# Performance work log

Measured on AMD Instinct MI355X. Metric: run time of the kernel, lower is better.

Reference implementation:

```python
import jax, jax.numpy as jnp
import numpy as np

E, TOP_K = 8, 2          # num_experts, num_experts_per_tok
B, S, H, I = 4, 2048, 1024, 4096  # batch, seq, hidden, intermediate
STD = 0.02


def setup_inputs() -> dict:
    key = jax.random.key(0)
    k0, k1, k2, k3 = jax.random.split(key, 4)
    return {
        "x": jax.random.normal(k0, (B, S, H), jnp.float32),
        "w_gate": jax.random.normal(k1, (E, H), jnp.float32) * STD,                 # gate: Linear(H->E, no bias)
        "w_fc": jax.random.normal(k2, (E, I, H), jnp.float32) * STD,                # c_fc per-expert [E, out, in]
        "b_fc": jnp.zeros((E, I), jnp.float32),
        "w_proj": jax.random.normal(k3, (E, H, I), jnp.float32) * (STD / np.sqrt(2 * 24)),  # c_proj, n_layer=24 init scale
        "b_proj": jnp.zeros((E, H), jnp.float32),
    }


def reference(x, w_gate, w_fc, b_fc, w_proj, b_proj):
    b, s, h = x.shape
    xf = x.reshape(-1, h)                       # [T, H], T = B*S
    T = xf.shape[0]

    # --- routing (softmax in fp32, top-k, renormalize) ---
    router_logits = xf @ w_gate.T               # [T, E]
    probs = jax.nn.softmax(router_logits.astype(jnp.float32), axis=-1)
    top_w, top_idx = jax.lax.top_k(probs, TOP_K)            # [T, K]
    top_w = top_w / jnp.sum(top_w, axis=-1, keepdims=True)  # normalize_expert_weights
    top_w = top_w.astype(x.dtype)

    # combine[t, e] = gate weight of expert e for token t (0 if not selected)
    combine = jnp.zeros((T, E), x.dtype).at[jnp.arange(T)[:, None], top_idx].add(top_w)

    # --- experts: weighted sum of per-expert MLPs (same math as sort/gather/scatter) ---
    out = jnp.zeros_like(xf)
    for e in range(E):
        ht = jax.nn.gelu(xf @ w_fc[e].T + b_fc[e], approximate=False)  # [T, I]
        ht = ht @ w_proj[e].T + b_proj[e]                              # [T, H]
        out = out + combine[:, e:e + 1] * ht

    return out.reshape(b, s, h), router_logits
```

## Files before the change

### kernel.cpp

```cpp
#include <hip/hip_runtime.h>
#include <hip/hip_bf16.h>
#include <math.h>

#define T_TOK 8192
#define HID 1024
#define IDIM 4096
#define NE 8
#define TK (T_TOK*2)

typedef __attribute__((ext_vector_type(8))) short short8;
typedef __attribute__((ext_vector_type(4))) float f32x4;

__device__ __forceinline__ void gld_lds16(const void* g, void* l)
{
    __builtin_amdgcn_global_load_lds(
        (const __attribute__((address_space(1))) void*)g,
        (__attribute__((address_space(3))) void*)l, 16, 0, 0);
}

__global__ __launch_bounds__(256) void cvt_kernel(const float* __restrict__ src,
                                                  __hip_bfloat16* __restrict__ dst, int n4)
{
    int i = blockIdx.x * 256 + threadIdx.x;
    int stride = gridDim.x * 256;
    for (; i < n4; i += stride) {
        float4 v = ((const float4*)src)[i];
        union { __hip_bfloat16 h[4]; ushort4 u; } t;
        t.h[0] = __float2bfloat16(v.x);
        t.h[1] = __float2bfloat16(v.y);
        t.h[2] = __float2bfloat16(v.z);
        t.h[3] = __float2bfloat16(v.w);
        ((ushort4*)dst)[i] = t.u;
    }
}

__global__ __launch_bounds__(256) void router_kernel(const float* __restrict__ x,
                                                     const float* __restrict__ wg,
                                                     float* __restrict__ logits_out,
                                                     int* __restrict__ top_idx,
                                                     float* __restrict__ top_w,
                                                     int* __restrict__ counts)
{
    int wave = threadIdx.x >> 6, lane = threadIdx.x & 63;
    int t = blockIdx.x * 4 + wave;
    const float* xr = x + (size_t)t * HID;
    float acc[NE];
#pragma unroll
    for (int e = 0; e < NE; e++) acc[e] = 0.f;
    for (int h = lane; h < HID; h += 64) {
        float xv = xr[h];
#pragma unroll
        for (int e = 0; e < NE; e++) acc[e] += xv * wg[e * HID + h];
    }
#pragma unroll
    for (int e = 0; e < NE; e++)
        for (int off = 32; off > 0; off >>= 1)
            acc[e] += __shfl_down(acc[e], off, 64);
    if (lane == 0) {
        float mx = acc[0];
        for (int e = 1; e < NE; e++) mx = fmaxf(mx, acc[e]);
        float p[NE]; float s = 0.f;
        for (int e = 0; e < NE; e++) { p[e] = expf(acc[e] - mx); s += p[e]; }
        for (int e = 0; e < NE; e++) logits_out[(size_t)t * NE + e] = acc[e];
        int i1 = 0;
        for (int e = 1; e < NE; e++) if (p[e] > p[i1]) i1 = e;
        int i2 = -1;
        for (int e = 0; e < NE; e++) { if (e == i1) continue; if (i2 < 0 || p[e] > p[i2]) i2 = e; }
        float w1 = p[i1], w2 = p[i2], sw = w1 + w2;
        top_idx[t * 2] = i1; top_idx[t * 2 + 1] = i2;
        top_w[t * 2] = w1 / sw; top_w[t * 2 + 1] = w2 / sw;
        atomicAdd(&counts[i1], 1);
        atomicAdd(&counts[i2], 1);
    }
}

__global__ void scan_kernel(const int* __restrict__ counts, int* __restrict__ offsets)
{
    if (threadIdx.x == 0) {
        int s = 0;
        for (int e = 0; e < NE; e++) { offsets[e] = s; s += counts[e]; }
        offsets[NE] = s;
    }
}

__global__ __launch_bounds__(256) void scatter_kernel(const int* __restrict__ top_idx,
                                                      const float* __restrict__ top_w,
                                                      const int* __restrict__ offsets,
                                                      int* __restrict__ counts2,
                                                      int* __restrict__ expert_tok,
                                                      float* __restrict__ slot_w,
                                                      int* __restrict__ slot_of)
{
    int t = blockIdx.x * 256 + threadIdx.x;
    if (t >= T_TOK) return;
    for (int k = 0; k < 2; k++) {
        int e = top_idx[t * 2 + k];
        int pos = atomicAdd(&counts2[e], 1);
        int slot = offsets[e] + pos;
        expert_tok[slot] = t;
        slot_w[slot] = top_w[t * 2 + k];
        slot_of[t * 2 + k] = slot;
    }
}

__global__ __launch_bounds__(256) void gather_kernel(const float* __restrict__ x,
                                                     const int* __restrict__ expert_tok,
                                                     __hip_bfloat16* __restrict__ xg)
{
    int slot = blockIdx.x;
    int tok = expert_tok[slot];
    const float4* src = (const float4*)(x + (size_t)tok * HID);
    ushort4* dst = (ushort4*)(xg + (size_t)slot * HID);
    int h = threadIdx.x;
    float4 v = src[h];
    union { __hip_bfloat16 h4[4]; ushort4 u; } t;
    t.h4[0] = __float2bfloat16(v.x);
    t.h4[1] = __float2bfloat16(v.y);
    t.h4[2] = __float2bfloat16(v.z);
    t.h4[3] = __float2bfloat16(v.w);
    dst[h] = t.u;
}

template <int KDIM>
__device__ __forceinline__ void moe_gemm_loop(const __hip_bfloat16* __restrict__ A,
                                              int m0, int cnt,
                                              const __hip_bfloat16* __restrict__ B,
                                              __hip_bfloat16* Alds, __hip_bfloat16* Blds,
                                              f32x4 (&acc)[4][4])
{
    const int tid = threadIdx.x;
    const int lane = tid & 63, wave = tid >> 6;
    const int wt = (wave & 1) * 64, wn = (wave >> 1) * 64;
    const int fm = lane & 15, q = lane >> 4;
    const int csw = (q ^ ((fm >> 1) & 3)) * 8;

    const int srow = wave * 32 + (lane >> 2);
    const int cg = ((lane & 3) ^ ((lane >> 3) & 3)) * 8;
    int ra0 = m0 + srow;      ra0 = (ra0 < cnt) ? ra0 : (cnt - 1);
    int ra1 = m0 + srow + 16; ra1 = (ra1 < cnt) ? ra1 : (cnt - 1);
    const __hip_bfloat16* gA0 = A + (size_t)ra0 * KDIM + cg;
    const __hip_bfloat16* gA1 = A + (size_t)ra1 * KDIM + cg;
    const __hip_bfloat16* gB0 = B + (size_t)srow * KDIM + cg;
    const __hip_bfloat16* gB1 = B + (size_t)(srow + 16) * KDIM + cg;
    __hip_bfloat16* lA0 = Alds + (wave * 32) * 32;
    __hip_bfloat16* lA1 = lA0 + 16 * 32;
    __hip_bfloat16* lB0 = Blds + (wave * 32) * 32;
    __hip_bfloat16* lB1 = lB0 + 16 * 32;

    for (int kt = 0; kt < KDIM / 32; ++kt) {
        __syncthreads();
        gld_lds16(gA0, lA0); gld_lds16(gA1, lA1);
        gld_lds16(gB0, lB0); gld_lds16(gB1, lB1);
        gA0 += 32; gA1 += 32; gB0 += 32; gB1 += 32;
        __syncthreads();

        short8 tf[4], wf[4];
#pragma unroll
        for (int mi = 0; mi < 4; mi++)
            tf[mi] = *(const short8*)&Alds[(wt + mi * 16 + fm) * 32 + csw];
#pragma unroll
        for (int ni = 0; ni < 4; ni++)
            wf[ni] = *(const short8*)&Blds[(wn + ni * 16 + fm) * 32 + csw];
#pragma unroll
        for (int mi = 0; mi < 4; mi++)
#pragma unroll
            for (int ni = 0; ni < 4; ni++)
                acc[mi][ni] = __builtin_amdgcn_mfma_f32_16x16x32_bf16(
                    wf[ni], tf[mi], acc[mi][ni], 0, 0, 0);
    }
}

__global__ __launch_bounds__(256) void gemm_fc_kernel(const __hip_bfloat16* __restrict__ xg,
                                                      const __hip_bfloat16* __restrict__ wfc,
                                                      const float* __restrict__ b_fc,
                                                      const int* __restrict__ offsets,
                                                      __hip_bfloat16* __restrict__ ht)
{
    __shared__ __hip_bfloat16 Alds[128 * 32];
    __shared__ __hip_bfloat16 Blds[128 * 32];
    const int e = blockIdx.z;
    const int off = offsets[e];
    const int cnt = offsets[e + 1] - off;
    const int m0 = blockIdx.y * 128;
    if (m0 >= cnt) return;
    const int n0 = blockIdx.x * 128;

    f32x4 acc[4][4] = {};
    moe_gemm_loop<HID>(xg + (size_t)off * HID, m0, cnt,
                       wfc + (size_t)e * IDIM * HID + (size_t)n0 * HID, Alds, Blds, acc);

    const int tid = threadIdx.x, lane = tid & 63, wave = tid >> 6;
    const int wt = (wave & 1) * 64, wn = (wave >> 1) * 64, fm = lane & 15, q = lane >> 4;
#pragma unroll
    for (int mi = 0; mi < 4; mi++) {
        int m = m0 + wt + mi * 16 + fm;
        if (m >= cnt) continue;
        __hip_bfloat16* row = ht + (size_t)(off + m) * IDIM + n0 + wn;
#pragma unroll
        for (int ni = 0; ni < 4; ni++) {
            int nb = ni * 16 + q * 4;
            float4 bias = *(const float4*)&b_fc[(size_t)e * IDIM + n0 + wn + nb];
            union { __hip_bfloat16 h[4]; ushort4 u; } t;
#pragma unroll
            for (int r = 0; r < 4; r++) {
                float v = acc[mi][ni][r] + ((const float*)&bias)[r];
                t.h[r] = __float2bfloat16(0.5f * v * (1.0f + erff(v * 0.70710678118654752f)));
            }
            *(ushort4*)&row[nb] = t.u;
        }
    }
}

__global__ __launch_bounds__(256) void gemm_proj_kernel(const __hip_bfloat16* __restrict__ ht,
                                                        const __hip_bfloat16* __restrict__ wproj,
                                                        const float* __restrict__ b_proj,
                                                        const int* __restrict__ offsets,
                                                        const float* __restrict__ slot_w,
                                                        __hip_bfloat16* __restrict__ contrib)
{
    __shared__ __hip_bfloat16 Alds[128 * 32];
    __shared__ __hip_bfloat16 Blds[128 * 32];
    const int f = blockIdx.x;
    const int x = f & 7, j = (f >> 3) & 7, H = f >> 6;
    const int G = H * 8 + x;
    const int e = G >> 6, mb = G & 63, nbk = j;
    const int off = offsets[e];
    const int cnt = offsets[e + 1] - off;
    const int m0 = mb * 128;
    if (m0 >= cnt) return;
    const int n0 = nbk * 128;

    f32x4 acc[4][4] = {};
    moe_gemm_loop<IDIM>(ht + (size_t)off * IDIM, m0, cnt,
                        wproj + (size_t)e * HID * IDIM + (size_t)n0 * IDIM, Alds, Blds, acc);

    const int tid = threadIdx.x, lane = tid & 63, wave = tid >> 6;
    const int wt = (wave & 1) * 64, wn = (wave >> 1) * 64, fm = lane & 15, q = lane >> 4;
#pragma unroll
    for (int mi = 0; mi < 4; mi++) {
        int m = m0 + wt + mi * 16 + fm;
        if (m >= cnt) continue;
        float sw = slot_w[off + m];
        __hip_bfloat16* row = contrib + (size_t)(off + m) * HID + n0 + wn;
#pragma unroll
        for (int ni = 0; ni < 4; ni++) {
            int nb = ni * 16 + q * 4;
            float4 bias = *(const float4*)&b_proj[(size_t)e * HID + n0 + wn + nb];
            union { __hip_bfloat16 h[4]; ushort4 u; } t;
#pragma unroll
            for (int r = 0; r < 4; r++) {
                float v = (acc[mi][ni][r] + ((const float*)&bias)[r]) * sw;
                t.h[r] = __float2bfloat16(v);
            }
            *(ushort4*)&row[nb] = t.u;
        }
    }
}

__global__ __launch_bounds__(256) void combine_kernel(const __hip_bfloat16* __restrict__ contrib,
                                                      const int* __restrict__ slot_of,
                                                      float* __restrict__ out)
{
    int t = blockIdx.x;
    int s0 = slot_of[t * 2], s1 = slot_of[t * 2 + 1];
    const ushort4* c0 = (const ushort4*)(contrib + (size_t)s0 * HID);
    const ushort4* c1 = (const ushort4*)(contrib + (size_t)s1 * HID);
    float4* o = (float4*)(out + (size_t)t * HID);
    int h = threadIdx.x;
    ushort4 a = c0[h], b = c1[h];
    union { unsigned u; float f; } f0, f1, f2, f3, g0, g1, g2, g3;
    f0.u = ((unsigned)a.x << 16); f1.u = ((unsigned)a.y << 16);
    f2.u = ((unsigned)a.z << 16); f3.u = ((unsigned)a.w << 16);
    g0.u = ((unsigned)b.x << 16); g1.u = ((unsigned)b.y << 16);
    g2.u = ((unsigned)b.z << 16); g3.u = ((unsigned)b.w << 16);
    float4 r;
    r.x = f0.f + g0.f; r.y = f1.f + g1.f; r.z = f2.f + g2.f; r.w = f3.f + g3.f;
    o[h] = r;
}

extern "C" void kernel_launch(void* const* d_in, const int* in_sizes, int n_in,
                              void* d_out, int out_size, void* d_ws, size_t ws_size,
                              hipStream_t stream)
{
    const float* x      = (const float*)d_in[0];
    const float* w_gate = (const float*)d_in[1];
    const float* w_fc   = (const float*)d_in[2];
    const float* b_fc   = (const float*)d_in[3];
    const float* w_proj = (const float*)d_in[4];
    const float* b_proj = (const float*)d_in[5];
    float* out = (float*)d_out;
    float* logits_out = out + (size_t)T_TOK * HID;

    char* ws = (char*)d_ws;
    const size_t WB = (size_t)NE * IDIM * HID * 2;
    size_t o_wfc     = 0;
    size_t o_wproj   = o_wfc + WB;
    size_t o_xg      = o_wproj + WB;
    size_t o_ht      = o_xg + (size_t)TK * HID * 2;
    size_t o_contrib = o_ht + (size_t)TK * IDIM * 2;
    size_t o_route   = o_contrib + (size_t)TK * HID * 2;

    __hip_bfloat16* wfc_b   = (__hip_bfloat16*)(ws + o_wfc);
    __hip_bfloat16* wproj_b = (__hip_bfloat16*)(ws + o_wproj);
    __hip_bfloat16* xg      = (__hip_bfloat16*)(ws + o_xg);
    __hip_bfloat16* ht      = (__hip_bfloat16*)(ws + o_ht);
    __hip_bfloat16* contrib = (__hip_bfloat16*)(ws + o_contrib);

    size_t ro = o_route;
    int*   top_idx    = (int*)(ws + ro);   ro += (size_t)T_TOK * 2 * 4;
    float* top_w      = (float*)(ws + ro); ro += (size_t)T_TOK * 2 * 4;
    int*   counts     = (int*)(ws + ro);   ro += NE * 4;
    int*   counts2    = (int*)(ws + ro);   ro += NE * 4;
    int*   offsets    = (int*)(ws + ro);   ro += 16 * 4;
    int*   expert_tok = (int*)(ws + ro);   ro += (size_t)TK * 4;
    float* slot_w     = (float*)(ws + ro); ro += (size_t)TK * 4;
    int*   slot_of    = (int*)(ws + ro);   ro += (size_t)T_TOK * 2 * 4;

    if (ws_size < ro) return;

    hipMemsetAsync(counts, 0, 2 * NE * sizeof(int), stream);

    const int n4 = NE * IDIM * HID / 4;
    cvt_kernel<<<2048, 256, 0, stream>>>(w_fc, wfc_b, n4);
    cvt_kernel<<<2048, 256, 0, stream>>>(w_proj, wproj_b, n4);

    router_kernel<<<T_TOK / 4, 256, 0, stream>>>(x, w_gate, logits_out, top_idx, top_w, counts);
    scan_kernel<<<1, 64, 0, stream>>>(counts, offsets);
    scatter_kernel<<<T_TOK / 256, 256, 0, stream>>>(top_idx, top_w, offsets, counts2,
                                                    expert_tok, slot_w, slot_of);
    gather_kernel<<<TK, 256, 0, stream>>>(x, expert_tok, xg);

    gemm_fc_kernel<<<dim3(IDIM / 128, T_TOK / 128, NE), 256, 0, stream>>>(
        xg, wfc_b, b_fc, offsets, ht);
    gemm_proj_kernel<<<NE * 64 * 8, 256, 0, stream>>>(
        ht, wproj_b, b_proj, offsets, slot_w, contrib);

    combine_kernel<<<T_TOK, 256, 0, stream>>>(contrib, slot_of, out);
}
```

Measured before the change: 1.068 ms.

## Fuse weight conversion and scatter/gather, double K-step in GEMMs, fast GELU

Merges the two weight-conversion launches into one kernel and fuses the scatter and gather kernels so each token row is read once and written to both expert slots. The GEMM main loop now loads 64 K-elements per barrier pair instead of 32, halving synchronisation count at the cost of doubled LDS per block. The exact erf GELU is replaced by an Abramowitz-Stegun polynomial approximation with hardware rcp/exp2, and bias loads are hoisted out of the epilogue loops. The GELU approximation has error around 1e-7 relative, which is below bf16 output precision.

```diff
diff --git a/kernel.cpp b/kernel.cpp
--- a/kernel.cpp
+++ b/kernel.cpp
@@ -18,19 +18,39 @@
         (__attribute__((address_space(3))) void*)l, 16, 0, 0);
 }
 
-__global__ __launch_bounds__(256) void cvt_kernel(const float* __restrict__ src,
-                                                  __hip_bfloat16* __restrict__ dst, int n4)
+__device__ __forceinline__ float fast_gelu(float v)
+{
+    float ax = fabsf(v) * 0.70710678118654752f;
+    float t = __builtin_amdgcn_rcpf(__builtin_fmaf(0.3275911f, ax, 1.0f));
+    float p = __builtin_fmaf(1.061405429f, t, -1.453152027f);
+    p = __builtin_fmaf(p, t, 1.421413741f);
+    p = __builtin_fmaf(p, t, -0.284496736f);
+    p = __builtin_fmaf(p, t, 0.254829592f);
+    p = p * t;
+    float ex = __builtin_amdgcn_exp2f(-ax * ax * 1.4426950408889634f);
+    float er = __builtin_fmaf(-p, ex, 1.0f);
+    er = copysignf(er, v);
+    return 0.5f * v * (1.0f + er);
+}
+
+__global__ __launch_bounds__(256) void cvt2_kernel(const float* __restrict__ a,
+                                                   __hip_bfloat16* __restrict__ da,
+                                                   const float* __restrict__ b,
+                                                   __hip_bfloat16* __restrict__ db, int n4)
 {
     int i = blockIdx.x * 256 + threadIdx.x;
     int stride = gridDim.x * 256;
-    for (; i < n4; i += stride) {
-        float4 v = ((const float4*)src)[i];
+    for (; i < 2 * n4; i += stride) {
+        const float4* s; ushort4* d; int j;
+        if (i < n4) { s = (const float4*)a; d = (ushort4*)da; j = i; }
+        else        { s = (const float4*)b; d = (ushort4*)db; j = i - n4; }
+        float4 v = s[j];
         union { __hip_bfloat16 h[4]; ushort4 u; } t;
         t.h[0] = __float2bfloat16(v.x);
         t.h[1] = __float2bfloat16(v.y);
         t.h[2] = __float2bfloat16(v.z);
         t.h[3] = __float2bfloat16(v.w);
-        ((ushort4*)dst)[i] = t.u;
+        d[j] = t.u;
     }
 }
 
@@ -83,42 +103,38 @@
     }
 }
 
-__global__ __launch_bounds__(256) void scatter_kernel(const int* __restrict__ top_idx,
-                                                      const float* __restrict__ top_w,
-                                                      const int* __restrict__ offsets,
-                                                      int* __restrict__ counts2,
-                                                      int* __restrict__ expert_tok,
-                                                      float* __restrict__ slot_w,
-                                                      int* __restrict__ slot_of)
-{
-    int t = blockIdx.x * 256 + threadIdx.x;
-    if (t >= T_TOK) return;
-    for (int k = 0; k < 2; k++) {
-        int e = top_idx[t * 2 + k];
-        int pos = atomicAdd(&counts2[e], 1);
-        int slot = offsets[e] + pos;
-        expert_tok[slot] = t;
-        slot_w[slot] = top_w[t * 2 + k];
-        slot_of[t * 2 + k] = slot;
-    }
-}
-
-__global__ __launch_bounds__(256) void gather_kernel(const float* __restrict__ x,
-                                                     const int* __restrict__ expert_tok,
-                                                     __hip_bfloat16* __restrict__ xg)
-{
-    int slot = blockIdx.x;
-    int tok = expert_tok[slot];
-    const float4* src = (const float4*)(x + (size_t)tok * HID);
-    ushort4* dst = (ushort4*)(xg + (size_t)slot * HID);
-    int h = threadIdx.x;
-    float4 v = src[h];
-    union { __hip_bfloat16 h4[4]; ushort4 u; } t;
-    t.h4[0] = __float2bfloat16(v.x);
-    t.h4[1] = __float2bfloat16(v.y);
-    t.h4[2] = __float2bfloat16(v.z);
-    t.h4[3] = __float2bfloat16(v.w);
-    dst[h] = t.u;
+__global__ __launch_bounds__(256) void scatter_gather_kernel(const float* __restrict__ x,
+                                                             const int* __restrict__ top_idx,
+                                                             const float* __restrict__ top_w,
+                                                             const int* __restrict__ offsets,
+                                                             int* __restrict__ counts2,
+                                                             float* __restrict__ slot_w,
+                                                             int* __restrict__ slot_of,
+                                                             __hip_bfloat16* __restrict__ xg)
+{
+    __shared__ int s_slot[2];
+    int t = blockIdx.x;
+    if (threadIdx.x == 0) {
+#pragma unroll
+        for (int k = 0; k < 2; k++) {
+            int e = top_idx[t * 2 + k];
+            int pos = atomicAdd(&counts2[e], 1);
+            int slot = offsets[e] + pos;
+            s_slot[k] = slot;
+            slot_w[slot] = top_w[t * 2 + k];
+            slot_of[t * 2 + k] = slot;
+        }
+    }
+    __syncthreads();
+    int s0 = s_slot[0], s1 = s_slot[1];
+    float4 v = ((const float4*)(x + (size_t)t * HID))[threadIdx.x];
+    union { __hip_bfloat16 h4[4]; ushort4 u; } c;
+    c.h4[0] = __float2bfloat16(v.x);
+    c.h4[1] = __float2bfloat16(v.y);
+    c.h4[2] = __float2bfloat16(v.z);
+    c.h4[3] = __float2bfloat16(v.w);
+    ((ushort4*)(xg + (size_t)s0 * HID))[threadIdx.x] = c.u;
+    ((ushort4*)(xg + (size_t)s1 * HID))[threadIdx.x] = c.u;
 }
 
 template <int KDIM>
@@ -133,6 +149,7 @@
     const int wt = (wave & 1) * 64, wn = (wave >> 1) * 64;
     const int fm = lane & 15, q = lane >> 4;
     const int csw = (q ^ ((fm >> 1) & 3)) * 8;
+    const int SUB = 128 * 32;
 
     const int srow = wave * 32 + (lane >> 2);
     const int cg = ((lane & 3) ^ ((lane >> 3) & 3)) * 8;
@@ -147,26 +164,30 @@
     __hip_bfloat16* lB0 = Blds + (wave * 32) * 32;
     __hip_bfloat16* lB1 = lB0 + 16 * 32;
 
-    for (int kt = 0; kt < KDIM / 32; ++kt) {
+    for (int kt = 0; kt < KDIM / 64; ++kt) {
         __syncthreads();
-        gld_lds16(gA0, lA0); gld_lds16(gA1, lA1);
-        gld_lds16(gB0, lB0); gld_lds16(gB1, lB1);
-        gA0 += 32; gA1 += 32; gB0 += 32; gB1 += 32;
+        gld_lds16(gA0, lA0);      gld_lds16(gA0 + 32, lA0 + SUB);
+        gld_lds16(gA1, lA1);      gld_lds16(gA1 + 32, lA1 + SUB);
+        gld_lds16(gB0, lB0);      gld_lds16(gB0 + 32, lB0 + SUB);
+        gld_lds16(gB1, lB1);      gld_lds16(gB1 + 32, lB1 + SUB);
+        gA0 += 64; gA1 += 64; gB0 += 64; gB1 += 64;
         __syncthreads();
-
-        short8 tf[4], wf[4];
-#pragma unroll
-        for (int mi = 0; mi < 4; mi++)
-            tf[mi] = *(const short8*)&Alds[(wt + mi * 16 + fm) * 32 + csw];
-#pragma unroll
-        for (int ni = 0; ni < 4; ni++)
-            wf[ni] = *(const short8*)&Blds[(wn + ni * 16 + fm) * 32 + csw];
-#pragma unroll
-        for (int mi = 0; mi < 4; mi++)
+#pragma unroll
+        for (int h = 0; h < 2; ++h) {
+            short8 tf[4], wf[4];
+#pragma unroll
+            for (int mi = 0; mi < 4; mi++)
+                tf[mi] = *(const short8*)&Alds[h * SUB + (wt + mi * 16 + fm) * 32 + csw];
 #pragma unroll
             for (int ni = 0; ni < 4; ni++)
-                acc[mi][ni] = __builtin_amdgcn_mfma_f32_16x16x32_bf16(
-                    wf[ni], tf[mi], acc[mi][ni], 0, 0, 0);
+                wf[ni] = *(const short8*)&Blds[h * SUB + (wn + ni * 16 + fm) * 32 + csw];
+#pragma unroll
+            for (int mi = 0; mi < 4; mi++)
+#pragma unroll
+                for (int ni = 0; ni < 4; ni++)
+                    acc[mi][ni] = __builtin_amdgcn_mfma_f32_16x16x32_bf16(
+                        wf[ni], tf[mi], acc[mi][ni], 0, 0, 0);
+        }
     }
 }
 
@@ -176,8 +197,8 @@
                                                       const int* __restrict__ offsets,
                                                       __hip_bfloat16* __restrict__ ht)
 {
-    __shared__ __hip_bfloat16 Alds[128 * 32];
-    __shared__ __hip_bfloat16 Blds[128 * 32];
+    __shared__ __hip_bfloat16 Alds[2 * 128 * 32];
+    __shared__ __hip_bfloat16 Blds[2 * 128 * 32];
     const int e = blockIdx.z;
     const int off = offsets[e];
     const int cnt = offsets[e + 1] - off;
@@ -191,6 +212,10 @@
 
     const int tid = threadIdx.x, lane = tid & 63, wave = tid >> 6;
     const int wt = (wave & 1) * 64, wn = (wave >> 1) * 64, fm = lane & 15, q = lane >> 4;
+    float4 bias4[4];
+#pragma unroll
+    for (int ni = 0; ni < 4; ni++)
+        bias4[ni] = *(const float4*)&b_fc[(size_t)e * IDIM + n0 + wn + ni * 16 + q * 4];
 #pragma unroll
     for (int mi = 0; mi < 4; mi++) {
         int m = m0 + wt + mi * 16 + fm;
@@ -199,12 +224,11 @@
 #pragma unroll
         for (int ni = 0; ni < 4; ni++) {
             int nb = ni * 16 + q * 4;
-            float4 bias = *(const float4*)&b_fc[(size_t)e * IDIM + n0 + wn + nb];
             union { __hip_bfloat16 h[4]; ushort4 u; } t;
 #pragma unroll
             for (int r = 0; r < 4; r++) {
-                float v = acc[mi][ni][r] + ((const float*)&bias)[r];
-                t.h[r] = __float2bfloat16(0.5f * v * (1.0f + erff(v * 0.70710678118654752f)));
+                float v = acc[mi][ni][r] + ((const float*)&bias4[ni])[r];
+                t.h[r] = __float2bfloat16(fast_gelu(v));
             }
             *(ushort4*)&row[nb] = t.u;
         }
@@ -218,11 +242,11 @@
                                                         const float* __restrict__ slot_w,
                                                         __hip_bfloat16* __restrict__ contrib)
 {
-    __shared__ __hip_bfloat16 Alds[128 * 32];
-    __shared__ __hip_bfloat16 Blds[128 * 32];
+    __shared__ __hip_bfloat16 Alds[2 * 128 * 32];
+    __shared__ __hip_bfloat16 Blds[2 * 128 * 32];
     const int f = blockIdx.x;
-    const int x = f & 7, j = (f >> 3) & 7, H = f >> 6;
-    const int G = H * 8 + x;
+    const int xs = f & 7, j = (f >> 3) & 7, H = f >> 6;
+    const int G = H * 8 + xs;
     const int e = G >> 6, mb = G & 63, nbk = j;
     const int off = offsets[e];
     const int cnt = offsets[e + 1] - off;
@@ -236,6 +260,10 @@
 
     const int tid = threadIdx.x, lane = tid & 63, wave = tid >> 6;
     const int wt = (wave & 1) * 64, wn = (wave >> 1) * 64, fm = lane & 15, q = lane >> 4;
+    float4 bias4[4];
+#pragma unroll
+    for (int ni = 0; ni < 4; ni++)
+        bias4[ni] = *(const float4*)&b_proj[(size_t)e * HID + n0 + wn + ni * 16 + q * 4];
 #pragma unroll
     for (int mi = 0; mi < 4; mi++) {
         int m = m0 + wt + mi * 16 + fm;
@@ -245,11 +273,10 @@
 #pragma unroll
         for (int ni = 0; ni < 4; ni++) {
             int nb = ni * 16 + q * 4;
-            float4 bias = *(const float4*)&b_proj[(size_t)e * HID + n0 + wn + nb];
             union { __hip_bfloat16 h[4]; ushort4 u; } t;
 #pragma unroll
             for (int r = 0; r < 4; r++) {
-                float v = (acc[mi][ni][r] + ((const float*)&bias)[r]) * sw;
+                float v = (acc[mi][ni][r] + ((const float*)&bias4[ni])[r]) * sw;
                 t.h[r] = __float2bfloat16(v);
             }
             *(ushort4*)&row[nb] = t.u;
@@ -312,7 +339,6 @@
     int*   counts     = (int*)(ws + ro);   ro += NE * 4;
     int*   counts2    = (int*)(ws + ro);   ro += NE * 4;
     int*   offsets    = (int*)(ws + ro);   ro += 16 * 4;
-    int*   expert_tok = (int*)(ws + ro);   ro += (size_t)TK * 4;
     float* slot_w     = (float*)(ws + ro); ro += (size_t)TK * 4;
     int*   slot_of    = (int*)(ws + ro);   ro += (size_t)T_TOK * 2 * 4;
 
@@ -321,14 +347,12 @@
     hipMemsetAsync(counts, 0, 2 * NE * sizeof(int), stream);
 
     const int n4 = NE * IDIM * HID / 4;
-    cvt_kernel<<<2048, 256, 0, stream>>>(w_fc, wfc_b, n4);
-    cvt_kernel<<<2048, 256, 0, stream>>>(w_proj, wproj_b, n4);
+    cvt2_kernel<<<4096, 256, 0, stream>>>(w_fc, wfc_b, w_proj, wproj_b, n4);
 
     router_kernel<<<T_TOK / 4, 256, 0, stream>>>(x, w_gate, logits_out, top_idx, top_w, counts);
     scan_kernel<<<1, 64, 0, stream>>>(counts, offsets);
-    scatter_kernel<<<T_TOK / 256, 256, 0, stream>>>(top_idx, top_w, offsets, counts2,
-                                                    expert_tok, slot_w, slot_of);
-    gather_kernel<<<TK, 256, 0, stream>>>(x, expert_tok, xg);
+    scatter_gather_kernel<<<T_TOK, 256, 0, stream>>>(x, top_idx, top_w, offsets, counts2,
+                                                     slot_w, slot_of, xg);
 
     gemm_fc_kernel<<<dim3(IDIM / 128, T_TOK / 128, NE), 256, 0, stream>>>(
         xg, wfc_b, b_fc, offsets, ht);
```

After: 1.197 ms. 12.1% more time.
